# Kernel optimization log

Hardware: AMD Instinct MI355X
Metric: run time of the kernel (lower is better)

The kernel has to match this reference:

```python
import jax, jax.numpy as jnp
import numpy as np

NUM_EMBEDDINGS = 2048
EMBEDDING_DIM = 512
INPUT_DIM = 256  # input_chan**2 = 16**2
COMMITMENT_COST = 0.25
BN_EPS = 1e-5


def setup_inputs() -> dict:
    key = jax.random.key(0)
    ks = jax.random.split(key, 8)
    B, N = 64, 1024
    inputs = jax.random.normal(ks[0], (B, N, INPUT_DIM), dtype=jnp.float32)
    # embedding init: uniform(-1/K, 1/K) as in the torch module
    emb_scale = 1.0 / NUM_EMBEDDINGS
    embedding = jax.random.uniform(ks[1], (NUM_EMBEDDINGS, EMBEDDING_DIM), dtype=jnp.float32,
                                   minval=-emb_scale, maxval=emb_scale)
    # Linear layers use torch convention W[out, in]
    W1 = jax.random.normal(ks[2], (EMBEDDING_DIM, INPUT_DIM), dtype=jnp.float32) / np.sqrt(INPUT_DIM)
    b1 = jnp.zeros((EMBEDDING_DIM,), dtype=jnp.float32)
    W2 = jax.random.normal(ks[3], (INPUT_DIM, EMBEDDING_DIM), dtype=jnp.float32) / np.sqrt(EMBEDDING_DIM)
    b2 = jnp.zeros((INPUT_DIM,), dtype=jnp.float32)
    # BatchNorm affine params initialized to 1/0 as in the module
    bn1_gamma = jnp.ones((INPUT_DIM,), dtype=jnp.float32)
    bn1_beta = jnp.zeros((INPUT_DIM,), dtype=jnp.float32)
    bn2_gamma = jnp.ones((EMBEDDING_DIM,), dtype=jnp.float32)
    bn2_beta = jnp.zeros((EMBEDDING_DIM,), dtype=jnp.float32)
    return {"inputs": inputs, "bn1_gamma": bn1_gamma, "bn1_beta": bn1_beta,
            "W1": W1, "b1": b1, "embedding": embedding,
            "bn2_gamma": bn2_gamma, "bn2_beta": bn2_beta, "W2": W2, "b2": b2}


def reference(inputs, bn1_gamma, bn1_beta, W1, b1, embedding, bn2_gamma, bn2_beta, W2, b2):
    sg = jax.lax.stop_gradient
    input_shape = inputs.shape
    flat = inputs.reshape(-1, INPUT_DIM)  # [T, D_in]
    # BatchNorm1d in eval mode (running_mean=0, running_var=1); Dropout is identity in eval.
    bn1_scale = 1.0 / jnp.sqrt(1.0 + BN_EPS)
    x = flat * (bn1_gamma * bn1_scale) + bn1_beta
    x = x @ W1.T + b1  # [T, E]
    # pairwise squared distances to codebook, argmin
    distances = (jnp.sum(x * x, axis=1, keepdims=True)
                 + jnp.sum(embedding * embedding, axis=1)
                 - 2.0 * x @ embedding.T)  # [T, K]
    encoding_indices = jnp.argmin(distances, axis=1)  # [T]
    # gather == one-hot @ embedding (same math, same gradient scatter-add)
    quantized = jnp.take(embedding, encoding_indices, axis=0)  # [T, E]
    bn2_scale = 1.0 / jnp.sqrt(1.0 + BN_EPS)
    quantized = quantized * (bn2_gamma * bn2_scale) + bn2_beta
    quantized = (quantized @ W2.T + b2).reshape(input_shape)
    e_latent_loss = jnp.mean((sg(quantized) - inputs) ** 2)
    q_latent_loss = jnp.mean((quantized - sg(inputs)) ** 2)
    loss = q_latent_loss + COMMITMENT_COST * e_latent_loss
    quantized_st = inputs + sg(quantized - inputs)  # straight-through
    T = flat.shape[0]
    usage = jnp.zeros((NUM_EMBEDDINGS,), dtype=jnp.float32).at[encoding_indices].add(1.0) / T
    return (loss, quantized_st, usage)
```

## Files before the change

kernel.cpp:

```cpp
#include <hip/hip_runtime.h>
#include <math.h>
#include <stdint.h>

#define TOK 65536
#define DIN 256
#define EDIM 512
#define KCB 2048
#define NTB 128

#define OFF_MP   0u
#define OFF_CP   524288u
#define OFF_Q    526336u
#define OFF_W2T  1050624u
#define OFF_U    1181696u
#define OFF_CQ   1182208u
#define OFF_BH   1182464u
#define TOT_F    1444608u

typedef short short8 __attribute__((ext_vector_type(8)));
typedef float f32x4 __attribute__((ext_vector_type(4)));

__device__ __forceinline__ unsigned short bf16rne(float x) {
    uint32_t u = __float_as_uint(x);
    u += 0x7fffu + ((u >> 16) & 1u);
    return (unsigned short)(u >> 16);
}
__device__ __forceinline__ void async_load16(const void* g, void* l) {
    __builtin_amdgcn_global_load_lds((const __attribute__((address_space(1))) void*)g,
                                     (__attribute__((address_space(3))) void*)l, 16, 0, 0);
}

__global__ void prep1_kernel(const float* __restrict__ W1, const float* __restrict__ W2,
                             const float* __restrict__ bn1_beta, const float* __restrict__ bn2_gamma,
                             const float* __restrict__ bn2_beta, const float* __restrict__ b2,
                             float* __restrict__ W2T, float* __restrict__ u, float* __restrict__ cQ,
                             float* __restrict__ out) {
    __shared__ float red[256];
    const int b = blockIdx.x, t = threadIdx.x;
    const int gid = b * 256 + t;
    if (gid == 0) out[0] = 0.0f;
    if (gid < KCB) out[1 + TOK * DIN + gid] = 0.0f;
    const float s = 1.0f / sqrtf(1.0f + 1e-5f);
    if (b < EDIM) {
        int e = b;
        W2T[e * DIN + t] = bn2_gamma[e] * s * W2[t * EDIM + e];
        float v = bn1_beta[t] * W1[e * DIN + t];
        red[t] = v; __syncthreads();
        for (int off = 128; off; off >>= 1) { if (t < off) red[t] += red[t + off]; __syncthreads(); }
        if (t == 0) u[e] = red[0];
    } else {
        int o = b - EDIM;
        float v = bn2_beta[t] * W2[o * EDIM + t] + bn2_beta[t + 256] * W2[o * EDIM + t + 256];
        red[t] = v; __syncthreads();
        for (int off = 128; off; off >>= 1) { if (t < off) red[t] += red[t + off]; __syncthreads(); }
        if (t == 0) cQ[o] = b2[o] + red[0];
    }
}

__global__ __launch_bounds__(256) void prep2_kernel(const float* __restrict__ E, const float* __restrict__ W1,
                                                    const float* __restrict__ W2T, const float* __restrict__ bn1_gamma,
                                                    const float* __restrict__ cQ, const float* __restrict__ b1,
                                                    const float* __restrict__ u,
                                                    float* __restrict__ Mp, float* __restrict__ Q,
                                                    float* __restrict__ cp) {
    __shared__ float Elds[4 * EDIM];
    const int k0 = blockIdx.x * 4, t = threadIdx.x;
    const float4* src = (const float4*)(E + (size_t)k0 * EDIM);
    float4* dst = (float4*)Elds;
    dst[t] = src[t];
    dst[256 + t] = src[256 + t];
    __syncthreads();
    float m[4] = {0, 0, 0, 0};
    float q[4] = {0, 0, 0, 0};
    for (int e0 = 0; e0 < EDIM; e0 += 8) {
        float w1v[8], w2v[8];
#pragma unroll
        for (int j = 0; j < 8; j++) {
            w1v[j] = W1[(e0 + j) * DIN + t];
            w2v[j] = W2T[(e0 + j) * DIN + t];
        }
#pragma unroll
        for (int j = 0; j < 8; j++) {
#pragma unroll
            for (int r = 0; r < 4; r++) {
                float ev = Elds[r * EDIM + e0 + j];
                m[r] += ev * w1v[j]; q[r] += ev * w2v[j];
            }
        }
    }
    const float s = 1.0f / sqrtf(1.0f + 1e-5f);
    const float gs = bn1_gamma[t] * s;
    const float cq = cQ[t];
#pragma unroll
    for (int r = 0; r < 4; r++) {
        Mp[(size_t)(k0 + r) * DIN + t] = gs * m[r];
        Q[(size_t)(k0 + r) * DIN + t] = q[r] + cq;
    }
    const int r = t >> 6, l = t & 63;
    float sa = 0.0f, sb = 0.0f;
#pragma unroll
    for (int i = 0; i < 8; i++) {
        int e = l + i * 64;
        float ev = Elds[r * EDIM + e];
        float be = b1[e] + u[e];
        sa += ev * be; sb += ev * ev;
    }
    float v = sa - 0.5f * sb;
#pragma unroll
    for (int off = 32; off; off >>= 1) v += __shfl_down(v, off, 64);
    if (l == 0) cp[k0 + r] = v;
}

__global__ __launch_bounds__(256) void packB_kernel(const float* __restrict__ Mp,
                                                    unsigned short* __restrict__ Bh) {
    __shared__ __align__(16) unsigned short Hs[32 * 264];
    const int t = threadIdx.x, lane = t & 63, w = t >> 6;
    const int r0 = blockIdx.x * 32;
    const float4* src = (const float4*)(Mp + (size_t)r0 * DIN);
#pragma unroll
    for (int i = 0; i < 8; i++) {
        int id = i * 256 + t;
        int row = id >> 6, c4 = id & 63;
        float4 v = src[id];
        float f[4] = {v.x, v.y, v.z, v.w};
        ushort4 H;
        unsigned short* hp = (unsigned short*)&H;
#pragma unroll
        for (int j = 0; j < 4; j++) hp[j] = bf16rne(f[j]);
        *(ushort4*)&Hs[row * 264 + c4 * 4] = H;
    }
    __syncthreads();
#pragma unroll
    for (int q = 0; q < 4; q++) {
        int fb = q * 4 + w;
        int tl = fb >> 3, kc = fb & 7;
        int srow = tl * 16 + (lane & 15);
        int scol = kc * 32 + (lane >> 4) * 8;
        short8 vh = *(const short8*)&Hs[srow * 264 + scol];
        size_t off = ((size_t)kc * NTB + (r0 >> 4) + tl) * 512 + lane * 8;
        *(short8*)&Bh[off] = vh;
    }
}

__global__ __launch_bounds__(256) void score_fused_kernel(const float* __restrict__ flat,
                                                          const unsigned short* __restrict__ Bh,
                                                          const float* __restrict__ cp,
                                                          const float* __restrict__ Q,
                                                          float* __restrict__ out) {
    __shared__ __align__(16) unsigned short Blds[2][32 * 512];
    __shared__ int ksel[128];
    const int t = threadIdx.x, lane = t & 63, w = t >> 6;
    const int m0 = blockIdx.x * 128;
    const int fr = lane & 15, qr = lane >> 4;

    short8 af[8][2];
#pragma unroll
    for (int kc = 0; kc < 8; kc++)
#pragma unroll
        for (int mt = 0; mt < 2; mt++) {
            int row = m0 + w * 32 + mt * 16 + fr;
            const float* p = flat + (size_t)row * DIN + kc * 32 + qr * 8;
            float4 a = *(const float4*)p;
            float4 b = *(const float4*)(p + 4);
            float f[8] = {a.x, a.y, a.z, a.w, b.x, b.y, b.z, b.w};
            unsigned short* hp = (unsigned short*)&af[kc][mt];
#pragma unroll
            for (int j = 0; j < 8; j++) hp[j] = bf16rne(f[j]);
        }

#pragma unroll
    for (int i = 0; i < 8; i++) {
        int tl = i * 4 + w;
        int kc = tl >> 2, nt = tl & 3;
        async_load16(Bh + ((size_t)kc * NTB + nt) * 512 + lane * 8,
                     &Blds[0][tl * 512 + lane * 8]);
    }
    __syncthreads();

    float bestv[2][4];
    int besti[2][4];
#pragma unroll
    for (int mt = 0; mt < 2; mt++)
#pragma unroll
        for (int r = 0; r < 4; r++) { bestv[mt][r] = -3.4e38f; besti[mt][r] = 0; }

    const f32x4 ZERO4 = {0.f, 0.f, 0.f, 0.f};

#pragma unroll 1
    for (int s = 0; s < 32; s++) {
        const int cur = s & 1;
        if (s < 31) {
            const int nxt = cur ^ 1;
#pragma unroll
            for (int i = 0; i < 8; i++) {
                int tl = i * 4 + w;
                int kc = tl >> 2, nt = tl & 3;
                async_load16(Bh + ((size_t)kc * NTB + (s + 1) * 4 + nt) * 512 + lane * 8,
                             &Blds[nxt][tl * 512 + lane * 8]);
            }
        }
        f32x4 acc[2][4];
        {
            short8 bf[4];
#pragma unroll
            for (int nt = 0; nt < 4; nt++)
                bf[nt] = *(const short8*)&Blds[cur][nt * 512 + lane * 8];
#pragma unroll
            for (int mt = 0; mt < 2; mt++)
#pragma unroll
                for (int nt = 0; nt < 4; nt++)
                    acc[mt][nt] = __builtin_amdgcn_mfma_f32_16x16x32_bf16(af[0][mt], bf[nt], ZERO4, 0, 0, 0);
        }
#pragma unroll
        for (int kc = 1; kc < 8; kc++) {
            short8 bf[4];
#pragma unroll
            for (int nt = 0; nt < 4; nt++)
                bf[nt] = *(const short8*)&Blds[cur][(kc * 4 + nt) * 512 + lane * 8];
#pragma unroll
            for (int mt = 0; mt < 2; mt++)
#pragma unroll
                for (int nt = 0; nt < 4; nt++)
                    acc[mt][nt] = __builtin_amdgcn_mfma_f32_16x16x32_bf16(af[kc][mt], bf[nt], acc[mt][nt], 0, 0, 0);
        }
        const int base = s * 64 + fr;
        float cpv[4];
        int cidx[4];
#pragma unroll
        for (int nt = 0; nt < 4; nt++) { cpv[nt] = cp[base + nt * 16]; cidx[nt] = base + nt * 16; }
#pragma unroll
        for (int mt = 0; mt < 2; mt++)
#pragma unroll
            for (int r = 0; r < 4; r++) {
                float v = acc[mt][0][r] + cpv[0];
                int ci = cidx[0];
#pragma unroll
                for (int nt = 1; nt < 4; nt++) {
                    float vi = acc[mt][nt][r] + cpv[nt];
                    if (vi > v) { v = vi; ci = cidx[nt]; }
                }
                if (v > bestv[mt][r]) { bestv[mt][r] = v; besti[mt][r] = ci; }
            }
        __syncthreads();
    }

#pragma unroll
    for (int mt = 0; mt < 2; mt++)
#pragma unroll
        for (int r = 0; r < 4; r++) {
            float bv = bestv[mt][r];
            int bc = besti[mt][r];
#pragma unroll
            for (int xm = 1; xm < 16; xm <<= 1) {
                float ov = __shfl_xor(bv, xm, 64);
                int oc = __shfl_xor(bc, xm, 64);
                if (ov > bv || (ov == bv && oc < bc)) { bv = ov; bc = oc; }
            }
            if (fr == 0) ksel[w * 32 + mt * 16 + qr * 4 + r] = bc;
        }
    __syncthreads();

    float lsum = 0.0f;
    for (int rr = 0; rr < 32; rr++) {
        int rl = w * 32 + rr;
        int row = m0 + rl;
        int k = ksel[rl];
        const float* qr_ = Q + (size_t)k * DIN;
        const float* xr = flat + (size_t)row * DIN;
        float* ob = out + 1 + (size_t)row * DIN;
#pragma unroll
        for (int cc = 0; cc < 4; cc++) {
            int j = lane + 64 * cc;
            float q = qr_[j];
            float d = q - xr[j];
            lsum += d * d;
            ob[j] = q;
        }
        if (lane == 0) atomicAdd(out + 1 + TOK * DIN + k, 1.0f / (float)TOK);
    }
#pragma unroll
    for (int off = 32; off; off >>= 1) lsum += __shfl_down(lsum, off, 64);
    if (lane == 0) atomicAdd(out, lsum * (1.25f / (float)((size_t)TOK * DIN)));
}

extern "C" void kernel_launch(void* const* d_in, const int* in_sizes, int n_in,
                              void* d_out, int out_size, void* d_ws, size_t ws_size,
                              hipStream_t stream) {
    const float* inputs = (const float*)d_in[0];
    const float* bn1_gamma = (const float*)d_in[1];
    const float* bn1_beta  = (const float*)d_in[2];
    const float* W1 = (const float*)d_in[3];
    const float* b1 = (const float*)d_in[4];
    const float* E  = (const float*)d_in[5];
    const float* bn2_gamma = (const float*)d_in[6];
    const float* bn2_beta  = (const float*)d_in[7];
    const float* W2 = (const float*)d_in[8];
    const float* b2 = (const float*)d_in[9];

    float* ws = (float*)d_ws;
    float* Mp  = ws + OFF_MP;
    float* cp  = ws + OFF_CP;
    float* Q   = ws + OFF_Q;
    float* W2T = ws + OFF_W2T;
    float* u   = ws + OFF_U;
    float* cQ  = ws + OFF_CQ;
    unsigned short* Bh = (unsigned short*)(ws + OFF_BH);
    float* out = (float*)d_out;

    hipLaunchKernelGGL(prep1_kernel, dim3(768), dim3(256), 0, stream,
                       W1, W2, bn1_beta, bn2_gamma, bn2_beta, b2, W2T, u, cQ, out);
    hipLaunchKernelGGL(prep2_kernel, dim3(512), dim3(256), 0, stream,
                       E, W1, W2T, bn1_gamma, cQ, b1, u, Mp, Q, cp);
    hipLaunchKernelGGL(packB_kernel, dim3(64), dim3(256), 0, stream, Mp, Bh);
    hipLaunchKernelGGL(score_fused_kernel, dim3(512), dim3(256), 0, stream,
                       inputs, Bh, cp, Q, out);
}
```

Measured before the change: 275.1 us.

## Deepen codebook staging to 4-buffer pipeline with split waitcnt and LDS bias

Restructures the score kernel's codebook streaming from a double-buffered 64-code stage into a four-buffer ring of 32-code stages, issued two stages ahead. It uses explicit vmcnt waits and a raw s_barrier per stage instead of a full __syncthreads, so global loads can overlap more compute. The codebook bias vector is staged into LDS once rather than read from global memory every iteration, and MFMA blocks run at raised wave priority. The cost is more barriers per tile and hand-tuned waitcnt counts that depend on how many async loads each stage issues.

```diff
diff --git a/kernel.cpp b/kernel.cpp
--- a/kernel.cpp
+++ b/kernel.cpp
@@ -147,7 +147,8 @@
                                                           const float* __restrict__ cp,
                                                           const float* __restrict__ Q,
                                                           float* __restrict__ out) {
-    __shared__ __align__(16) unsigned short Blds[2][32 * 512];
+    __shared__ __align__(16) unsigned short Blds[4][16 * 512];
+    __shared__ float cpl[KCB];
     __shared__ int ksel[128];
     const int t = threadIdx.x, lane = t & 63, w = t >> 6;
     const int m0 = blockIdx.x * 128;
@@ -168,14 +169,24 @@
             for (int j = 0; j < 8; j++) hp[j] = bf16rne(f[j]);
         }
 
-#pragma unroll
-    for (int i = 0; i < 8; i++) {
-        int tl = i * 4 + w;
-        int kc = tl >> 2, nt = tl & 3;
-        async_load16(Bh + ((size_t)kc * NTB + nt) * 512 + lane * 8,
-                     &Blds[0][tl * 512 + lane * 8]);
-    }
+    ((float4*)cpl)[t] = ((const float4*)cp)[t];
+    ((float4*)cpl)[256 + t] = ((const float4*)cp)[256 + t];
+
     __syncthreads();
+
+#define STAGE_ISSUE(sidx, bidx)                                                     \
+    do {                                                                            \
+        _Pragma("unroll")                                                           \
+        for (int i_ = 0; i_ < 4; i_++) {                                            \
+            int tl_ = i_ * 4 + w;                                                   \
+            int kc_ = tl_ >> 1, nt_ = tl_ & 1;                                      \
+            async_load16(Bh + ((size_t)kc_ * NTB + (sidx) * 2 + nt_) * 512 + lane * 8, \
+                         &Blds[bidx][tl_ * 512 + lane * 8]);                        \
+        }                                                                           \
+    } while (0)
+
+    STAGE_ISSUE(0, 0);
+    STAGE_ISSUE(1, 1);
 
     float bestv[2][4];
     int besti[2][4];
@@ -187,62 +198,58 @@
     const f32x4 ZERO4 = {0.f, 0.f, 0.f, 0.f};
 
 #pragma unroll 1
-    for (int s = 0; s < 32; s++) {
-        const int cur = s & 1;
-        if (s < 31) {
-            const int nxt = cur ^ 1;
-#pragma unroll
-            for (int i = 0; i < 8; i++) {
-                int tl = i * 4 + w;
-                int kc = tl >> 2, nt = tl & 3;
-                async_load16(Bh + ((size_t)kc * NTB + (s + 1) * 4 + nt) * 512 + lane * 8,
-                             &Blds[nxt][tl * 512 + lane * 8]);
-            }
-        }
-        f32x4 acc[2][4];
+    for (int s = 0; s < 64; s++) {
+        const int cur = s & 3;
+        if (s < 62) {
+            const int nb = (s + 2) & 3;
+            STAGE_ISSUE(s + 2, nb);
+            asm volatile("s_waitcnt vmcnt(8)" ::: "memory");
+        } else if (s == 62) {
+            asm volatile("s_waitcnt vmcnt(4)" ::: "memory");
+        } else {
+            asm volatile("s_waitcnt vmcnt(0)" ::: "memory");
+        }
+        __builtin_amdgcn_s_barrier();
+        __builtin_amdgcn_sched_barrier(0);
+
+        f32x4 acc[2][2];
+        __builtin_amdgcn_s_setprio(1);
         {
-            short8 bf[4];
-#pragma unroll
-            for (int nt = 0; nt < 4; nt++)
-                bf[nt] = *(const short8*)&Blds[cur][nt * 512 + lane * 8];
-#pragma unroll
-            for (int mt = 0; mt < 2; mt++)
-#pragma unroll
-                for (int nt = 0; nt < 4; nt++)
-                    acc[mt][nt] = __builtin_amdgcn_mfma_f32_16x16x32_bf16(af[0][mt], bf[nt], ZERO4, 0, 0, 0);
+            short8 bf0 = *(const short8*)&Blds[cur][0 * 512 + lane * 8];
+            short8 bf1 = *(const short8*)&Blds[cur][1 * 512 + lane * 8];
+#pragma unroll
+            for (int mt = 0; mt < 2; mt++) {
+                acc[mt][0] = __builtin_amdgcn_mfma_f32_16x16x32_bf16(af[0][mt], bf0, ZERO4, 0, 0, 0);
+                acc[mt][1] = __builtin_amdgcn_mfma_f32_16x16x32_bf16(af[0][mt], bf1, ZERO4, 0, 0, 0);
+            }
         }
 #pragma unroll
         for (int kc = 1; kc < 8; kc++) {
-            short8 bf[4];
-#pragma unroll
-            for (int nt = 0; nt < 4; nt++)
-                bf[nt] = *(const short8*)&Blds[cur][(kc * 4 + nt) * 512 + lane * 8];
-#pragma unroll
-            for (int mt = 0; mt < 2; mt++)
-#pragma unroll
-                for (int nt = 0; nt < 4; nt++)
-                    acc[mt][nt] = __builtin_amdgcn_mfma_f32_16x16x32_bf16(af[kc][mt], bf[nt], acc[mt][nt], 0, 0, 0);
-        }
-        const int base = s * 64 + fr;
-        float cpv[4];
-        int cidx[4];
-#pragma unroll
-        for (int nt = 0; nt < 4; nt++) { cpv[nt] = cp[base + nt * 16]; cidx[nt] = base + nt * 16; }
+            short8 bf0 = *(const short8*)&Blds[cur][(kc * 2 + 0) * 512 + lane * 8];
+            short8 bf1 = *(const short8*)&Blds[cur][(kc * 2 + 1) * 512 + lane * 8];
+#pragma unroll
+            for (int mt = 0; mt < 2; mt++) {
+                acc[mt][0] = __builtin_amdgcn_mfma_f32_16x16x32_bf16(af[kc][mt], bf0, acc[mt][0], 0, 0, 0);
+                acc[mt][1] = __builtin_amdgcn_mfma_f32_16x16x32_bf16(af[kc][mt], bf1, acc[mt][1], 0, 0, 0);
+            }
+        }
+        __builtin_amdgcn_s_setprio(0);
+
+        const int base = s * 32 + fr;
+        const float cpv0 = cpl[base];
+        const float cpv1 = cpl[base + 16];
 #pragma unroll
         for (int mt = 0; mt < 2; mt++)
 #pragma unroll
             for (int r = 0; r < 4; r++) {
-                float v = acc[mt][0][r] + cpv[0];
-                int ci = cidx[0];
-#pragma unroll
-                for (int nt = 1; nt < 4; nt++) {
-                    float vi = acc[mt][nt][r] + cpv[nt];
-                    if (vi > v) { v = vi; ci = cidx[nt]; }
-                }
+                float v0 = acc[mt][0][r] + cpv0;
+                float v1 = acc[mt][1][r] + cpv1;
+                float v = v0; int ci = base;
+                if (v1 > v0) { v = v1; ci = base + 16; }
                 if (v > bestv[mt][r]) { bestv[mt][r] = v; besti[mt][r] = ci; }
             }
-        __syncthreads();
-    }
+    }
+#undef STAGE_ISSUE
 
 #pragma unroll
     for (int mt = 0; mt < 2; mt++)
```

New measurement: 287.7 us. +4.6%, slower.

## Split score kernel rows across eight waves, cache code-bias in LDS, raise MFMA priority

Applied to the files above, without the earlier changes.

The fused score kernel now runs 512 threads per block. Each of the eight waves owns 16 token rows instead of 32, which halves the per-wave A fragments and accumulators. The codebook bias vector is staged into shared memory once per block rather than read from global memory on every step, and s_setprio raises wave priority around the MFMA section. The change aims to add more waves to hide LDS and global latency, at the cost of more B-tile LDS reads per MFMA (each B fragment now feeds one row tile instead of two) and more barrier participants.

```diff
diff --git a/kernel.cpp b/kernel.cpp
--- a/kernel.cpp
+++ b/kernel.cpp
@@ -142,47 +142,46 @@
     }
 }
 
-__global__ __launch_bounds__(256) void score_fused_kernel(const float* __restrict__ flat,
+__global__ __launch_bounds__(512) void score_fused_kernel(const float* __restrict__ flat,
                                                           const unsigned short* __restrict__ Bh,
                                                           const float* __restrict__ cp,
                                                           const float* __restrict__ Q,
                                                           float* __restrict__ out) {
     __shared__ __align__(16) unsigned short Blds[2][32 * 512];
+    __shared__ float cpl[KCB];
     __shared__ int ksel[128];
     const int t = threadIdx.x, lane = t & 63, w = t >> 6;
     const int m0 = blockIdx.x * 128;
     const int fr = lane & 15, qr = lane >> 4;
 
-    short8 af[8][2];
-#pragma unroll
-    for (int kc = 0; kc < 8; kc++)
-#pragma unroll
-        for (int mt = 0; mt < 2; mt++) {
-            int row = m0 + w * 32 + mt * 16 + fr;
-            const float* p = flat + (size_t)row * DIN + kc * 32 + qr * 8;
-            float4 a = *(const float4*)p;
-            float4 b = *(const float4*)(p + 4);
-            float f[8] = {a.x, a.y, a.z, a.w, b.x, b.y, b.z, b.w};
-            unsigned short* hp = (unsigned short*)&af[kc][mt];
-#pragma unroll
-            for (int j = 0; j < 8; j++) hp[j] = bf16rne(f[j]);
-        }
-
-#pragma unroll
-    for (int i = 0; i < 8; i++) {
-        int tl = i * 4 + w;
+    short8 af[8];
+#pragma unroll
+    for (int kc = 0; kc < 8; kc++) {
+        int row = m0 + w * 16 + fr;
+        const float* p = flat + (size_t)row * DIN + kc * 32 + qr * 8;
+        float4 a = *(const float4*)p;
+        float4 b = *(const float4*)(p + 4);
+        float f[8] = {a.x, a.y, a.z, a.w, b.x, b.y, b.z, b.w};
+        unsigned short* hp = (unsigned short*)&af[kc];
+#pragma unroll
+        for (int j = 0; j < 8; j++) hp[j] = bf16rne(f[j]);
+    }
+
+    ((float4*)cpl)[t] = ((const float4*)cp)[t];
+
+#pragma unroll
+    for (int i = 0; i < 4; i++) {
+        int tl = i * 8 + w;
         int kc = tl >> 2, nt = tl & 3;
         async_load16(Bh + ((size_t)kc * NTB + nt) * 512 + lane * 8,
                      &Blds[0][tl * 512 + lane * 8]);
     }
     __syncthreads();
 
-    float bestv[2][4];
-    int besti[2][4];
-#pragma unroll
-    for (int mt = 0; mt < 2; mt++)
-#pragma unroll
-        for (int r = 0; r < 4; r++) { bestv[mt][r] = -3.4e38f; besti[mt][r] = 0; }
+    float bestv[4];
+    int besti[4];
+#pragma unroll
+    for (int r = 0; r < 4; r++) { bestv[r] = -3.4e38f; besti[r] = 0; }
 
     const f32x4 ZERO4 = {0.f, 0.f, 0.f, 0.f};
 
@@ -192,24 +191,23 @@
         if (s < 31) {
             const int nxt = cur ^ 1;
 #pragma unroll
-            for (int i = 0; i < 8; i++) {
-                int tl = i * 4 + w;
+            for (int i = 0; i < 4; i++) {
+                int tl = i * 8 + w;
                 int kc = tl >> 2, nt = tl & 3;
                 async_load16(Bh + ((size_t)kc * NTB + (s + 1) * 4 + nt) * 512 + lane * 8,
                              &Blds[nxt][tl * 512 + lane * 8]);
             }
         }
-        f32x4 acc[2][4];
+        f32x4 acc[4];
+        __builtin_amdgcn_s_setprio(1);
         {
             short8 bf[4];
 #pragma unroll
             for (int nt = 0; nt < 4; nt++)
                 bf[nt] = *(const short8*)&Blds[cur][nt * 512 + lane * 8];
 #pragma unroll
-            for (int mt = 0; mt < 2; mt++)
-#pragma unroll
-                for (int nt = 0; nt < 4; nt++)
-                    acc[mt][nt] = __builtin_amdgcn_mfma_f32_16x16x32_bf16(af[0][mt], bf[nt], ZERO4, 0, 0, 0);
+            for (int nt = 0; nt < 4; nt++)
+                acc[nt] = __builtin_amdgcn_mfma_f32_16x16x32_bf16(af[0], bf[nt], ZERO4, 0, 0, 0);
         }
 #pragma unroll
         for (int kc = 1; kc < 8; kc++) {
@@ -218,51 +216,47 @@
             for (int nt = 0; nt < 4; nt++)
                 bf[nt] = *(const short8*)&Blds[cur][(kc * 4 + nt) * 512 + lane * 8];
 #pragma unroll
-            for (int mt = 0; mt < 2; mt++)
-#pragma unroll
-                for (int nt = 0; nt < 4; nt++)
-                    acc[mt][nt] = __builtin_amdgcn_mfma_f32_16x16x32_bf16(af[kc][mt], bf[nt], acc[mt][nt], 0, 0, 0);
-        }
+            for (int nt = 0; nt < 4; nt++)
+                acc[nt] = __builtin_amdgcn_mfma_f32_16x16x32_bf16(af[kc], bf[nt], acc[nt], 0, 0, 0);
+        }
+        __builtin_amdgcn_s_setprio(0);
+
         const int base = s * 64 + fr;
         float cpv[4];
         int cidx[4];
 #pragma unroll
-        for (int nt = 0; nt < 4; nt++) { cpv[nt] = cp[base + nt * 16]; cidx[nt] = base + nt * 16; }
-#pragma unroll
-        for (int mt = 0; mt < 2; mt++)
-#pragma unroll
-            for (int r = 0; r < 4; r++) {
-                float v = acc[mt][0][r] + cpv[0];
-                int ci = cidx[0];
-#pragma unroll
-                for (int nt = 1; nt < 4; nt++) {
-                    float vi = acc[mt][nt][r] + cpv[nt];
-                    if (vi > v) { v = vi; ci = cidx[nt]; }
-                }
-                if (v > bestv[mt][r]) { bestv[mt][r] = v; besti[mt][r] = ci; }
+        for (int nt = 0; nt < 4; nt++) { cpv[nt] = cpl[base + nt * 16]; cidx[nt] = base + nt * 16; }
+#pragma unroll
+        for (int r = 0; r < 4; r++) {
+            float v = acc[0][r] + cpv[0];
+            int ci = cidx[0];
+#pragma unroll
+            for (int nt = 1; nt < 4; nt++) {
+                float vi = acc[nt][r] + cpv[nt];
+                if (vi > v) { v = vi; ci = cidx[nt]; }
             }
+            if (v > bestv[r]) { bestv[r] = v; besti[r] = ci; }
+        }
         __syncthreads();
     }
 
 #pragma unroll
-    for (int mt = 0; mt < 2; mt++)
-#pragma unroll
-        for (int r = 0; r < 4; r++) {
-            float bv = bestv[mt][r];
-            int bc = besti[mt][r];
-#pragma unroll
-            for (int xm = 1; xm < 16; xm <<= 1) {
-                float ov = __shfl_xor(bv, xm, 64);
-                int oc = __shfl_xor(bc, xm, 64);
-                if (ov > bv || (ov == bv && oc < bc)) { bv = ov; bc = oc; }
-            }
-            if (fr == 0) ksel[w * 32 + mt * 16 + qr * 4 + r] = bc;
-        }
+    for (int r = 0; r < 4; r++) {
+        float bv = bestv[r];
+        int bc = besti[r];
+#pragma unroll
+        for (int xm = 1; xm < 16; xm <<= 1) {
+            float ov = __shfl_xor(bv, xm, 64);
+            int oc = __shfl_xor(bc, xm, 64);
+            if (ov > bv || (ov == bv && oc < bc)) { bv = ov; bc = oc; }
+        }
+        if (fr == 0) ksel[w * 16 + qr * 4 + r] = bc;
+    }
     __syncthreads();
 
     float lsum = 0.0f;
-    for (int rr = 0; rr < 32; rr++) {
-        int rl = w * 32 + rr;
+    for (int rr = 0; rr < 16; rr++) {
+        int rl = w * 16 + rr;
         int row = m0 + rl;
         int k = ksel[rl];
         const float* qr_ = Q + (size_t)k * DIN;
@@ -312,6 +306,6 @@
     hipLaunchKernelGGL(prep2_kernel, dim3(512), dim3(256), 0, stream,
                        E, W1, W2T, bn1_gamma, cQ, b1, u, Mp, Q, cp);
     hipLaunchKernelGGL(packB_kernel, dim3(64), dim3(256), 0, stream, Mp, Bh);
-    hipLaunchKernelGGL(score_fused_kernel, dim3(512), dim3(256), 0, stream,
+    hipLaunchKernelGGL(score_fused_kernel, dim3(512), dim3(512), 0, stream,
                        inputs, Bh, cp, Q, out);
 }
```

Result: slower. 319.4 us (+16.1%).

## Fuse bf16 packing of Mp into prep2 and drop packB kernel

Applied to the files above, without the earlier changes.

The prep2 kernel now handles 8 codebook rows per 512-thread block, converts the Mp projection straight to bf16 in shared memory, and writes it in the MFMA-tiled Bh layout. This removes the separate packB launch and the fp32 Mp round trip through global memory. Codebook values are now read directly from global memory (wave-uniform addresses) instead of being staged in LDS. The tile-layout index math must match the old packB mapping exactly, or the scores will be wrong.

```diff
diff --git a/kernel.cpp b/kernel.cpp
--- a/kernel.cpp
+++ b/kernel.cpp
@@ -57,88 +57,72 @@
     }
 }
 
-__global__ __launch_bounds__(256) void prep2_kernel(const float* __restrict__ E, const float* __restrict__ W1,
+__global__ __launch_bounds__(512) void prep2_kernel(const float* __restrict__ E, const float* __restrict__ W1,
                                                     const float* __restrict__ W2T, const float* __restrict__ bn1_gamma,
                                                     const float* __restrict__ cQ, const float* __restrict__ b1,
                                                     const float* __restrict__ u,
-                                                    float* __restrict__ Mp, float* __restrict__ Q,
-                                                    float* __restrict__ cp) {
-    __shared__ float Elds[4 * EDIM];
-    const int k0 = blockIdx.x * 4, t = threadIdx.x;
-    const float4* src = (const float4*)(E + (size_t)k0 * EDIM);
-    float4* dst = (float4*)Elds;
-    dst[t] = src[t];
-    dst[256 + t] = src[256 + t];
-    __syncthreads();
+                                                    float* __restrict__ Q, float* __restrict__ cp,
+                                                    unsigned short* __restrict__ Bh) {
+    __shared__ __align__(16) unsigned short hs[8][264];
+    const int t = threadIdx.x;
+    const int col = t & 255;
+    const int half = __builtin_amdgcn_readfirstlane(t >> 8);
+    const int k0 = blockIdx.x * 8;
+    const float* __restrict__ Ek = E + ((size_t)k0 + (size_t)half * 4) * EDIM;
+
     float m[4] = {0, 0, 0, 0};
     float q[4] = {0, 0, 0, 0};
     for (int e0 = 0; e0 < EDIM; e0 += 8) {
         float w1v[8], w2v[8];
 #pragma unroll
         for (int j = 0; j < 8; j++) {
-            w1v[j] = W1[(e0 + j) * DIN + t];
-            w2v[j] = W2T[(e0 + j) * DIN + t];
-        }
-#pragma unroll
-        for (int j = 0; j < 8; j++) {
-#pragma unroll
-            for (int r = 0; r < 4; r++) {
-                float ev = Elds[r * EDIM + e0 + j];
-                m[r] += ev * w1v[j]; q[r] += ev * w2v[j];
+            w1v[j] = W1[(e0 + j) * DIN + col];
+            w2v[j] = W2T[(e0 + j) * DIN + col];
+        }
+#pragma unroll
+        for (int r = 0; r < 4; r++) {
+#pragma unroll
+            for (int j = 0; j < 8; j++) {
+                float ev = Ek[(size_t)r * EDIM + e0 + j];
+                m[r] += ev * w1v[j];
+                q[r] += ev * w2v[j];
             }
         }
     }
     const float s = 1.0f / sqrtf(1.0f + 1e-5f);
-    const float gs = bn1_gamma[t] * s;
-    const float cq = cQ[t];
+    const float gs = bn1_gamma[col] * s;
+    const float cq = cQ[col];
 #pragma unroll
     for (int r = 0; r < 4; r++) {
-        Mp[(size_t)(k0 + r) * DIN + t] = gs * m[r];
-        Q[(size_t)(k0 + r) * DIN + t] = q[r] + cq;
-    }
-    const int r = t >> 6, l = t & 63;
-    float sa = 0.0f, sb = 0.0f;
-#pragma unroll
-    for (int i = 0; i < 8; i++) {
-        int e = l + i * 64;
-        float ev = Elds[r * EDIM + e];
-        float be = b1[e] + u[e];
-        sa += ev * be; sb += ev * ev;
-    }
-    float v = sa - 0.5f * sb;
-#pragma unroll
-    for (int off = 32; off; off >>= 1) v += __shfl_down(v, off, 64);
-    if (l == 0) cp[k0 + r] = v;
-}
-
-__global__ __launch_bounds__(256) void packB_kernel(const float* __restrict__ Mp,
-                                                    unsigned short* __restrict__ Bh) {
-    __shared__ __align__(16) unsigned short Hs[32 * 264];
-    const int t = threadIdx.x, lane = t & 63, w = t >> 6;
-    const int r0 = blockIdx.x * 32;
-    const float4* src = (const float4*)(Mp + (size_t)r0 * DIN);
-#pragma unroll
-    for (int i = 0; i < 8; i++) {
-        int id = i * 256 + t;
-        int row = id >> 6, c4 = id & 63;
-        float4 v = src[id];
-        float f[4] = {v.x, v.y, v.z, v.w};
-        ushort4 H;
-        unsigned short* hp = (unsigned short*)&H;
-#pragma unroll
-        for (int j = 0; j < 4; j++) hp[j] = bf16rne(f[j]);
-        *(ushort4*)&Hs[row * 264 + c4 * 4] = H;
-    }
+        Q[(size_t)(k0 + half * 4 + r) * DIN + col] = q[r] + cq;
+        hs[half * 4 + r][col] = bf16rne(gs * m[r]);
+    }
+
+    {
+        const int wv = t >> 6, l = t & 63;
+        const float* __restrict__ Er = E + (size_t)(k0 + wv) * EDIM;
+        float sa = 0.0f, sb = 0.0f;
+#pragma unroll
+        for (int i = 0; i < 8; i++) {
+            int e = l + i * 64;
+            float ev = Er[e];
+            float be = b1[e] + u[e];
+            sa += ev * be; sb += ev * ev;
+        }
+        float v = sa - 0.5f * sb;
+#pragma unroll
+        for (int off = 32; off; off >>= 1) v += __shfl_down(v, off, 64);
+        if (l == 0) cp[k0 + wv] = v;
+    }
+
     __syncthreads();
-#pragma unroll
-    for (int q = 0; q < 4; q++) {
-        int fb = q * 4 + w;
-        int tl = fb >> 3, kc = fb & 7;
-        int srow = tl * 16 + (lane & 15);
-        int scol = kc * 32 + (lane >> 4) * 8;
-        short8 vh = *(const short8*)&Hs[srow * 264 + scol];
-        size_t off = ((size_t)kc * NTB + (r0 >> 4) + tl) * 512 + lane * 8;
-        *(short8*)&Bh[off] = vh;
+
+    if (t < 256) {
+        const int rr = t & 7, qr = (t >> 3) & 3, kc = t >> 5;
+        const int nt = k0 >> 4;
+        const int l2 = (k0 & 8) + rr + (qr << 4);
+        short8 vh = *(const short8*)&hs[rr][kc * 32 + qr * 8];
+        *(short8*)&Bh[((size_t)kc * NTB + nt) * 512 + (size_t)l2 * 8] = vh;
     }
 }
 
@@ -298,7 +282,6 @@
     const float* b2 = (const float*)d_in[9];
 
     float* ws = (float*)d_ws;
-    float* Mp  = ws + OFF_MP;
     float* cp  = ws + OFF_CP;
     float* Q   = ws + OFF_Q;
     float* W2T = ws + OFF_W2T;
@@ -309,9 +292,8 @@
 
     hipLaunchKernelGGL(prep1_kernel, dim3(768), dim3(256), 0, stream,
                        W1, W2, bn1_beta, bn2_gamma, bn2_beta, b2, W2T, u, cQ, out);
-    hipLaunchKernelGGL(prep2_kernel, dim3(512), dim3(256), 0, stream,
-                       E, W1, W2T, bn1_gamma, cQ, b1, u, Mp, Q, cp);
-    hipLaunchKernelGGL(packB_kernel, dim3(64), dim3(256), 0, stream, Mp, Bh);
+    hipLaunchKernelGGL(prep2_kernel, dim3(256), dim3(512), 0, stream,
+                       E, W1, W2T, bn1_gamma, cQ, b1, u, Q, cp, Bh);
     hipLaunchKernelGGL(score_fused_kernel, dim3(512), dim3(256), 0, stream,
                        inputs, Bh, cp, Q, out);
 }
```

Measured after the change: 264.1 us. -4.0%, faster.
